# Kernel optimization log

Measured on AMD Instinct MI355X. Metric: run time of the kernel, lower is better.

The kernel has to match this reference:

```python
import jax, jax.numpy as jnp
import numpy as np

L, B, E = 512, 32, 512
ENC_HID, DEC_HID = 512, 1024
H2 = 2 * ENC_HID            # bidirectional encoder output dim
OUT_DIM = 32000             # generation (trg) vocab
CPY_LEN = 60000             # copy vocab size (embedding rows / prediction cols)
SRC_V = 50000
NEG = -1e10


def setup_inputs() -> dict:
    key = jax.random.key(0)
    ks = jax.random.split(key, 20)
    s = 0.02
    f32 = jnp.float32
    return {
        "src": jax.random.randint(ks[0], (L, B), 0, SRC_V),
        "inp": jax.random.randint(ks[1], (B,), 0, CPY_LEN),
        "hidden": jax.random.normal(ks[2], (2, B, DEC_HID), f32),
        "c": jax.random.normal(ks[3], (2, B, DEC_HID), f32),
        "encoder_outputs": jax.random.normal(ks[4], (L, B, H2), f32),
        "mask": jnp.ones((B, L), jnp.int32),
        "selective_weights": jax.random.normal(ks[5], (B, L - 2), f32),
        "src_to_cpy": jax.random.randint(ks[6], (SRC_V,), 0, CPY_LEN),
        # learned parameters
        "emb": jax.random.normal(ks[7], (CPY_LEN, E), f32) * s,
        "W_attn": jax.random.normal(ks[8], (H2 + DEC_HID, DEC_HID), f32) * s,
        "b_attn": jnp.zeros((DEC_HID,), f32),
        "v_attn": jax.random.normal(ks[9], (DEC_HID,), f32) * s,
        "W_ih0": jax.random.normal(ks[10], (4 * DEC_HID, 2 * H2 + E), f32) * s,
        "W_hh0": jax.random.normal(ks[11], (4 * DEC_HID, DEC_HID), f32) * s,
        "b_ih0": jnp.zeros((4 * DEC_HID,), f32),
        "b_hh0": jnp.zeros((4 * DEC_HID,), f32),
        "W_ih1": jax.random.normal(ks[12], (4 * DEC_HID, DEC_HID), f32) * s,
        "W_hh1": jax.random.normal(ks[13], (4 * DEC_HID, DEC_HID), f32) * s,
        "b_ih1": jnp.zeros((4 * DEC_HID,), f32),
        "b_hh1": jnp.zeros((4 * DEC_HID,), f32),
        "W_fc": jax.random.normal(ks[14], (OUT_DIM, H2 + DEC_HID + E), f32) * s,
        "b_fc": jnp.zeros((OUT_DIM,), f32),
        "W_copy": jax.random.normal(ks[15], (DEC_HID, H2), f32) * s,
        "b_copy": jnp.zeros((DEC_HID,), f32),
    }


def _lstm_cell(x, h, c, W_ih, W_hh, b_ih, b_hh):
    # PyTorch gate order: i, f, g, o
    g = x @ W_ih.T + h @ W_hh.T + b_ih + b_hh
    i, f, gg, o = jnp.split(g, 4, axis=-1)
    c_new = jax.nn.sigmoid(f) * c + jax.nn.sigmoid(i) * jnp.tanh(gg)
    h_new = jax.nn.sigmoid(o) * jnp.tanh(c_new)
    return h_new, c_new


def reference(src, inp, hidden, c, encoder_outputs, mask, selective_weights,
              src_to_cpy, emb, W_attn, b_attn, v_attn,
              W_ih0, W_hh0, b_ih0, b_hh0, W_ih1, W_hh1, b_ih1, b_hh1,
              W_fc, b_fc, W_copy, b_copy):
    Bn = encoder_outputs.shape[1]
    Ln = encoder_outputs.shape[0]
    # update_selective_weights: mask where converted src token != prev prediction, softmax
    conv_src = src_to_cpy[src[1:-1]]              # [L-2, B]
    copy_mask = (conv_src == inp[None, :]).T      # [B, L-2]
    sel = jnp.where(copy_mask, selective_weights, NEG)
    sel = jax.nn.softmax(sel, axis=1)             # [B, L-2]
    embedded = emb[inp]                           # [B, E] (dropout in eval mode = identity)
    enc = jnp.transpose(encoder_outputs, (1, 0, 2))  # [B, L, H2]
    # Bahdanau attention over encoder outputs
    h_top = hidden[-1]                            # [B, D]
    h_rep = jnp.broadcast_to(h_top[:, None, :], (Bn, Ln, h_top.shape[-1]))
    energy = jnp.tanh(jnp.concatenate([h_rep, enc], axis=2) @ W_attn + b_attn)  # [B, L, D]
    scores = energy @ v_attn                      # [B, L]
    scores = jnp.where(mask == 0, NEG, scores)
    attn_w = jax.nn.softmax(scores, axis=1)
    attentive_read = jnp.einsum('bl,blh->bh', attn_w, enc)        # [B, H2]
    sel = jnp.where(mask[:, 1:-1] == 0, NEG, sel)                 # faithful second mask
    selective_read = jnp.einsum('bl,blh->bh', sel, enc[:, 1:-1])  # [B, H2]
    # 2-layer LSTM, single step
    x = jnp.concatenate([embedded, attentive_read, selective_read], axis=1)
    h0, c0 = _lstm_cell(x, hidden[0], c[0], W_ih0, W_hh0, b_ih0, b_hh0)
    h1, c1 = _lstm_cell(h0, hidden[1], c[1], W_ih1, W_hh1, b_ih1, b_hh1)
    hidden_new = jnp.stack([h0, h1])
    c_new = jnp.stack([c0, c1])
    # generation scores
    gen = jnp.concatenate([h1, attentive_read, embedded], axis=1) @ W_fc.T + b_fc  # [B, OUT_DIM]
    # copy scores over trimmed source positions
    proj = jnp.tanh(enc[:, 1:-1] @ W_copy.T + b_copy)             # [B, L-2, D]
    copy_scores = jnp.einsum('bld,bd->bl', proj, h1)              # [B, L-2]
    copy_scores = jnp.where(mask[:, 1:-1] == 0, NEG, copy_scores)
    # assemble predictions: generation slice + indexed scatter of copy scores
    src_cpy = src_to_cpy[src.T[:, 1:-1]]                          # [B, L-2]
    preds = jnp.zeros((Bn, CPY_LEN), gen.dtype)
    preds = preds.at[:, :OUT_DIM].set(gen)
    preds = preds.at[jnp.arange(Bn)[:, None], src_cpy].set(copy_scores)
    return preds, hidden_new, c_new, attn_w, copy_scores
```

## Files before the change

### kernel.cpp

```cpp
#include <hip/hip_runtime.h>
#include <stdint.h>

typedef unsigned short u16;
typedef unsigned int   u32;
typedef __attribute__((ext_vector_type(8))) short short8;
typedef __attribute__((ext_vector_type(4))) float f32x4;

#define NEGF (-1.0e10f)

static constexpr int LL = 512, BB = 32, EE = 512, H2 = 1024, DH = 1024;
static constexpr int KX = 2560, OUTD = 32000, CPY = 60000;

static constexpr size_t HID_OFF   = 1920000;
static constexpr size_t C_OFF     = HID_OFF + 65536;
static constexpr size_t ATTN_OFF  = C_OFF + 65536;
static constexpr size_t CS_OFF    = ATTN_OFF + 16384;

static constexpr size_t WS_ENC    = 0;
static constexpr size_t WS_WA1T   = 33554432;
static constexpr size_t WS_WA2T   = 35651584;
static constexpr size_t WS_WCT    = 37748736;
static constexpr size_t WS_HPF    = 39845888;
static constexpr size_t WS_SCORES = 39976960;
static constexpr size_t WS_CSACC  = 40042496;
static constexpr size_t WS_SELP   = 40108032;
static constexpr size_t WS_XBF    = 40173568;
static constexpr size_t WS_GENBF  = 40337408;
static constexpr size_t WS_H0PBF  = 40501248;
static constexpr size_t WS_H1PBF  = 40566784;
static constexpr size_t WS_H0NBF  = 40632320;
static constexpr size_t WS_GATES  = 40697856;
static constexpr size_t WS_H1     = 41222144;
static constexpr size_t WS_TOTAL  = 41353216;
static constexpr size_t WS_GPART  = WS_WA1T;
static constexpr size_t WS_TAG    = WS_ENC;

__device__ __forceinline__ u16 f2bf(float x){
  u32 u = __builtin_bit_cast(u32, x);
  u32 r = (u + 0x7FFFu + ((u >> 16) & 1u)) >> 16;
  return (u16)r;
}
__device__ __forceinline__ float bf2f(u16 h){
  u32 u = ((u32)h) << 16; return __builtin_bit_cast(float, u);
}
__device__ __forceinline__ float fsig(float x){ return 1.f/(1.f + __expf(-x)); }
__device__ __forceinline__ float ftanh(float x){
  float e = __expf(2.f*x);
  return 1.f - 2.f/(e + 1.f);
}

#define GLDS16(gp, lp) __builtin_amdgcn_global_load_lds( \
    (__attribute__((address_space(1))) void*)(gp), \
    (__attribute__((address_space(3))) void*)(lp), 16, 0, 0)

__global__ void k_f32_to_bf16(const float* __restrict__ in, u16* __restrict__ out, int n4){
  int stride = gridDim.x * blockDim.x;
  for (int i = blockIdx.x*blockDim.x + threadIdx.x; i < n4; i += stride){
    float4 v = ((const float4*)in)[i];
    u32 lo = (u32)f2bf(v.x) | ((u32)f2bf(v.y) << 16);
    u32 hi = (u32)f2bf(v.z) | ((u32)f2bf(v.w) << 16);
    ((uint2*)out)[i] = make_uint2(lo, hi);
  }
}

__global__ void k_wattn_t(const float* __restrict__ W, u16* __restrict__ wa1t, u16* __restrict__ wa2t){
  __shared__ float Tt[64*65];
  int n0 = blockIdx.x*64, k0 = blockIdx.y*64;
  int t = threadIdx.x;
  int nn = t & 63, kq = t >> 6;
  for (int kk = kq; kk < 64; kk += 4)
    Tt[kk*65 + nn] = W[(size_t)(k0+kk)*1024 + n0 + nn];
  __syncthreads();
  u16* dst = (k0 < 1024) ? wa1t : wa2t;
  int kbase = (k0 < 1024) ? k0 : (k0 - 1024);
  int kk2 = t & 63, nq = t >> 6;
  for (int nn2 = nq; nn2 < 64; nn2 += 4)
    dst[(size_t)(n0+nn2)*1024 + kbase + kk2] = f2bf(Tt[kk2*65 + nn2]);
}

__global__ void k_prep(const int* __restrict__ src, const int* __restrict__ inp,
                       const float* __restrict__ hidden, const float* __restrict__ selw,
                       const int* __restrict__ s2c, const float* __restrict__ emb,
                       const int* __restrict__ mask,
                       u16* __restrict__ xbf, u16* __restrict__ genbf,
                       u16* __restrict__ h0pbf, u16* __restrict__ h1pbf,
                       float* __restrict__ scores, float* __restrict__ csacc,
                       float* __restrict__ selp)
{
  int b = blockIdx.x, t = threadIdx.x;
  int ib = inp[b];
  for (int h = t; h < 512; h += 256){
    u16 e = f2bf(emb[(size_t)ib*512 + h]);
    xbf[b*2560 + h] = e;
    genbf[b*2560 + 2048 + h] = e;
  }
  for (int k = t; k < 1024; k += 256){
    h0pbf[b*1024 + k] = f2bf(hidden[b*1024 + k]);
    h1pbf[b*1024 + k] = f2bf(hidden[32768 + b*1024 + k]);
  }
  for (int l = t; l < 512; l += 256){
    scores[b*512 + l] = 0.f;
    csacc[b*512 + l] = 0.f;
  }
  __shared__ float red[256];
  float lg[2];
  #pragma unroll
  for (int i = 0; i < 2; ++i){
    int j = t + i*256;
    lg[i] = NEGF;
    if (j < 510){
      int cs = s2c[src[(j+1)*32 + b]];
      if (cs == ib) lg[i] = selw[b*510 + j];
    }
  }
  red[t] = fmaxf(lg[0], lg[1]); __syncthreads();
  for (int s = 128; s > 0; s >>= 1){ if (t < s) red[t] = fmaxf(red[t], red[t+s]); __syncthreads(); }
  float mx = red[0]; __syncthreads();
  float e0 = (t < 510)     ? __expf(lg[0] - mx) : 0.f;
  float e1 = (t+256 < 510) ? __expf(lg[1] - mx) : 0.f;
  red[t] = e0 + e1; __syncthreads();
  for (int s = 128; s > 0; s >>= 1){ if (t < s) red[t] += red[t+s]; __syncthreads(); }
  float inv = 1.f / red[0];
  #pragma unroll
  for (int i = 0; i < 2; ++i){
    int j = t + i*256;
    if (j < 510){
      float v = ((i == 0) ? e0 : e1) * inv;
      int l = j + 1;
      selp[b*512 + l] = (mask[b*512 + l] != 0) ? v : NEGF;
    }
  }
}

__launch_bounds__(256)
__global__ void k_mfma(const u16* __restrict__ A, int lda, int Mvalid,
                       const u16* __restrict__ Bmat, int ldb, int K,
                       const float* __restrict__ preadd, int spa,
                       const float* __restrict__ dotw, int sdw,
                       float* __restrict__ dotout, int Ldot, int skipedge,
                       float* __restrict__ outstore, int NT)
{
  __shared__ u16 As[128*64];
  __shared__ u16 Bs[128*64];
  int nwg = gridDim.x, bid = blockIdx.x;
  int q = nwg >> 3, r = nwg & 7, xc = bid & 7, ix = bid >> 3;
  int wg = (xc < r ? xc*(q+1) : r*(q+1) + (xc - r)*q) + ix;
  int mt = wg / NT, nt = wg % NT;
  int m0 = mt * 128, n0 = nt * 128;
  int tid = threadIdx.x, lane = tid & 63, wid = tid >> 6;
  int wm = wid >> 1, wn = wid & 1;

  f32x4 acc[4][4];
  #pragma unroll
  for (int i = 0; i < 4; ++i)
    #pragma unroll
    for (int j = 0; j < 4; ++j)
      acc[i][j] = (f32x4){0.f, 0.f, 0.f, 0.f};

  int srow = lane >> 3;
  int soff = ((lane & 7) ^ srow) * 8;

  for (int k0 = 0; k0 < K; k0 += 64){
    __syncthreads();
    #pragma unroll
    for (int j = 0; j < 4; ++j){
      int qq = wid*4 + j;
      int ra = m0 + qq*8 + srow; if (ra >= Mvalid) ra = Mvalid - 1;
      GLDS16(A + (size_t)ra*lda + k0 + soff, (char*)As + qq*1024 + lane*16);
      int rb = n0 + qq*8 + srow;
      GLDS16(Bmat + (size_t)rb*ldb + k0 + soff, (char*)Bs + qq*1024 + lane*16);
    }
    __syncthreads();
    #pragma unroll
    for (int kk = 0; kk < 2; ++kk){
      short8 af[4], bfr[4];
      #pragma unroll
      for (int mi = 0; mi < 4; ++mi){
        int rr = wm*64 + mi*16 + (lane & 15);
        int kb = (kk*64 + ((lane >> 4) << 4)) ^ ((rr & 7) << 4);
        af[mi] = *(const short8*)((const char*)As + rr*128 + kb);
      }
      #pragma unroll
      for (int nj = 0; nj < 4; ++nj){
        int rr = wn*64 + nj*16 + (lane & 15);
        int kb = (kk*64 + ((lane >> 4) << 4)) ^ ((rr & 7) << 4);
        bfr[nj] = *(const short8*)((const char*)Bs + rr*128 + kb);
      }
      #pragma unroll
      for (int mi = 0; mi < 4; ++mi)
        #pragma unroll
        for (int nj = 0; nj < 4; ++nj)
          acc[mi][nj] = __builtin_amdgcn_mfma_f32_16x16x32_bf16(af[mi], bfr[nj], acc[mi][nj], 0, 0, 0);
    }
  }

  int g = lane >> 4, cn = lane & 15;
  if (outstore){
    int Nld = NT * 128;
    #pragma unroll
    for (int mi = 0; mi < 4; ++mi)
      #pragma unroll
      for (int rr2 = 0; rr2 < 4; ++rr2){
        int row = m0 + wm*64 + mi*16 + g*4 + rr2;
        if (row < Mvalid){
          #pragma unroll
          for (int nj = 0; nj < 4; ++nj){
            int n = n0 + wn*64 + nj*16 + cn;
            outstore[(size_t)row*Nld + n] = acc[mi][nj][rr2] + preadd[(size_t)(row & 31)*spa + n];
          }
        }
      }
  } else {
    #pragma unroll
    for (int mi = 0; mi < 4; ++mi)
      #pragma unroll
      for (int rr2 = 0; rr2 < 4; ++rr2){
        int row = m0 + wm*64 + mi*16 + g*4 + rr2;
        int bb = row & 31;
        float part = 0.f;
        #pragma unroll
        for (int nj = 0; nj < 4; ++nj){
          int n = n0 + wn*64 + nj*16 + cn;
          float tv = ftanh(acc[mi][nj][rr2] + preadd[(size_t)bb*spa + n]);
          part = fmaf(tv, dotw[(size_t)bb*sdw + n], part);
        }
        part += __shfl_xor(part, 1);
        part += __shfl_xor(part, 2);
        part += __shfl_xor(part, 4);
        part += __shfl_xor(part, 8);
        if (cn == 0){
          int l = row >> 5;
          if (!skipedge || (l > 0 && l < Ldot - 1))
            atomicAdd(&dotout[(size_t)bb*Ldot + l], part);
        }
      }
  }
}

__global__ void k_softmax_attn(const float* __restrict__ scores, const int* __restrict__ mask,
                               float* __restrict__ attnw){
  int b = blockIdx.x, t = threadIdx.x;
  __shared__ float red[256];
  float v0 = scores[b*512 + t];
  float v1 = scores[b*512 + 256 + t];
  if (mask[b*512 + t] == 0) v0 = NEGF;
  if (mask[b*512 + 256 + t] == 0) v1 = NEGF;
  red[t] = fmaxf(v0, v1); __syncthreads();
  for (int s = 128; s > 0; s >>= 1){ if (t < s) red[t] = fmaxf(red[t], red[t+s]); __syncthreads(); }
  float mx = red[0]; __syncthreads();
  float e0 = __expf(v0 - mx), e1 = __expf(v1 - mx);
  red[t] = e0 + e1; __syncthreads();
  for (int s = 128; s > 0; s >>= 1){ if (t < s) red[t] += red[t+s]; __syncthreads(); }
  float inv = 1.f / red[0];
  attnw[b*512 + t] = e0 * inv;
  attnw[b*512 + 256 + t] = e1 * inv;
}

__global__ void k_reads(const u16* __restrict__ encbf, const float* __restrict__ attnw,
                        const float* __restrict__ selp,
                        u16* __restrict__ xbf, u16* __restrict__ genbf){
  int b = blockIdx.y;
  int h = blockIdx.x*128 + threadIdx.x;
  float aa = 0.f, as = 0.f;
  #pragma unroll 4
  for (int l = 0; l < 512; ++l){
    float e = bf2f(encbf[((size_t)l*32 + b)*1024 + h]);
    aa = fmaf(attnw[b*512 + l], e, aa);
    if (l >= 1 && l < 511) as = fmaf(selp[b*512 + l], e, as);
  }
  u16 ab = f2bf(aa);
  xbf[b*2560 + 512 + h]  = ab;
  xbf[b*2560 + 1536 + h] = f2bf(as);
  genbf[b*2560 + 1024 + h] = ab;
}

__launch_bounds__(256)
__global__ void k_wgemm(const float* __restrict__ W1, const u16* __restrict__ xb1, int K1,
                        const float* __restrict__ W2, const u16* __restrict__ xb2, int K2,
                        const float* __restrict__ bias1, const float* __restrict__ bias2,
                        float* __restrict__ outB, int ldo, int cps)
{
  __shared__ u16 As[64*64];
  __shared__ u16 Bs[32*64];
  const int tid = threadIdx.x, lane = tid & 63, w = tid >> 6;
  const int o0 = blockIdx.x * 64;
  const int c1 = K1 >> 6;
  const int c0 = blockIdx.y * cps;

  f32x4 acc[2];
  acc[0] = (f32x4){0.f,0.f,0.f,0.f};
  acc[1] = (f32x4){0.f,0.f,0.f,0.f};

  const int ar = tid >> 2, akq = (tid & 3) * 16;
  const int aswz = (ar & 7) << 4;
  const int brow = tid >> 3, pslot = tid & 7;
  const int lslot = pslot ^ (brow & 7);

  float4 aA[4], aB[4];

  auto aload = [&](int c, float4* dst){
    const float* Wp; int Kp, kc;
    if (c < c1){ Wp = W1; Kp = K1; kc = c << 6; }
    else       { Wp = W2; Kp = K2; kc = (c - c1) << 6; }
    const float4* p = (const float4*)(Wp + (size_t)(o0 + ar)*Kp + kc + akq);
    dst[0] = p[0]; dst[1] = p[1]; dst[2] = p[2]; dst[3] = p[3];
  };

  auto body = [&](int c, float4* cur, float4* nxt, bool more){
    asm volatile("s_waitcnt lgkmcnt(0)" ::: "memory");
    __builtin_amdgcn_s_barrier();
    {
      const u16* xp; int Kp, kc;
      if (c < c1){ xp = xb1; Kp = K1; kc = c << 6; }
      else       { xp = xb2; Kp = K2; kc = (c - c1) << 6; }
      GLDS16(xp + (size_t)brow*Kp + kc + lslot*8, (char*)Bs + tid*16);
    }
    u32 p0 = (u32)f2bf(cur[0].x) | ((u32)f2bf(cur[0].y) << 16);
    u32 p1 = (u32)f2bf(cur[0].z) | ((u32)f2bf(cur[0].w) << 16);
    u32 p2 = (u32)f2bf(cur[1].x) | ((u32)f2bf(cur[1].y) << 16);
    u32 p3 = (u32)f2bf(cur[1].z) | ((u32)f2bf(cur[1].w) << 16);
    u32 p4 = (u32)f2bf(cur[2].x) | ((u32)f2bf(cur[2].y) << 16);
    u32 p5 = (u32)f2bf(cur[2].z) | ((u32)f2bf(cur[2].w) << 16);
    u32 p6 = (u32)f2bf(cur[3].x) | ((u32)f2bf(cur[3].y) << 16);
    u32 p7 = (u32)f2bf(cur[3].z) | ((u32)f2bf(cur[3].w) << 16);
    char* rowp = (char*)As + ar*128;
    *(uint4*)(rowp + ((akq*2)      ^ aswz)) = make_uint4(p0,p1,p2,p3);
    *(uint4*)(rowp + ((akq*2 + 16) ^ aswz)) = make_uint4(p4,p5,p6,p7);
    asm volatile("s_waitcnt lgkmcnt(0)\n\ts_waitcnt vmcnt(0)" ::: "memory");
    __builtin_amdgcn_s_barrier();
    if (more) aload(c + 1, nxt);
    #pragma unroll
    for (int kk = 0; kk < 2; ++kk){
      int rrA = w*16 + (lane & 15);
      int kb  = kk*64 + ((lane >> 4) << 4);
      short8 af = *(const short8*)((const char*)As + rrA*128 + (kb ^ ((rrA & 7) << 4)));
      #pragma unroll
      for (int nj = 0; nj < 2; ++nj){
        int rrB = nj*16 + (lane & 15);
        short8 bfv = *(const short8*)((const char*)Bs + rrB*128 + (kb ^ ((rrB & 7) << 4)));
        acc[nj] = __builtin_amdgcn_mfma_f32_16x16x32_bf16(af, bfv, acc[nj], 0, 0, 0);
      }
    }
  };

  aload(c0, aA);
  for (int li = 0; li < cps; li += 2){
    body(c0 + li,     aA, aB, true);
    body(c0 + li + 1, aB, aA, (li + 2) < cps);
  }

  int g = lane >> 4, cn = lane & 15;
  int ob = o0 + w*16 + g*4;
  float* outP = outB + (size_t)blockIdx.y * 32 * (size_t)ldo;
  float4 badd = make_float4(0.f,0.f,0.f,0.f);
  if (blockIdx.y == 0){
    if (bias1){ float4 t = *(const float4*)(bias1 + ob);
      badd.x += t.x; badd.y += t.y; badd.z += t.z; badd.w += t.w; }
    if (bias2){ float4 t = *(const float4*)(bias2 + ob);
      badd.x += t.x; badd.y += t.y; badd.z += t.z; badd.w += t.w; }
  }
  #pragma unroll
  for (int nj = 0; nj < 2; ++nj){
    int bcol = nj*16 + cn;
    float4 v = make_float4(acc[nj][0] + badd.x, acc[nj][1] + badd.y,
                           acc[nj][2] + badd.z, acc[nj][3] + badd.w);
    *(float4*)(outP + (size_t)bcol*ldo + ob) = v;
  }
}

__global__ void k_gred(const float* __restrict__ part, float* __restrict__ g){
  int i = blockIdx.x*256 + threadIdx.x;
  g[i] = part[i] + part[131072 + i] + part[262144 + i] + part[393216 + i];
}

__global__ void k_cell(const float* __restrict__ g, const float* __restrict__ c_in,
                       float* __restrict__ h_out, float* __restrict__ c_out,
                       u16* __restrict__ hbf, int hld, float* __restrict__ h_plain){
  int idx = blockIdx.x*256 + threadIdx.x;
  int b = idx >> 10, j = idx & 1023;
  const float* gb = g + (size_t)b*4096;
  float gi = gb[j];
  float gf = gb[1024 + j];
  float gg = gb[2048 + j];
  float go = gb[3072 + j];
  float cv = c_in[b*1024 + j];
  float cnv = fsig(gf)*cv + fsig(gi)*ftanh(gg);
  float hn  = fsig(go)*ftanh(cnv);
  c_out[b*1024 + j] = cnv;
  h_out[b*1024 + j] = hn;
  hbf[(size_t)b*hld + j] = f2bf(hn);
  if (h_plain) h_plain[b*1024 + j] = hn;
}

__global__ void k_zerotail(float* __restrict__ preds){
  int i = blockIdx.x*256 + threadIdx.x;
  if (i < 224000){
    int b = i / 7000, t = i % 7000;
    ((float4*)(preds + (size_t)b*CPY + OUTD))[t] = make_float4(0.f, 0.f, 0.f, 0.f);
  }
}

__global__ void k_csfinal(const float* __restrict__ csacc, const int* __restrict__ mask,
                          float* __restrict__ cs_out){
  int i = blockIdx.x*256 + threadIdx.x;
  if (i < 16320){
    int b = i / 510, j = i % 510, l = j + 1;
    cs_out[b*510 + j] = (mask[b*512 + l] != 0) ? csacc[b*512 + l] : NEGF;
  }
}

__global__ void k_tag_init(const int* __restrict__ src, const int* __restrict__ s2c,
                           int* __restrict__ tag){
  int i = blockIdx.x*256 + threadIdx.x;
  if (i < 16320){
    int b = i / 510, j = i % 510;
    tag[(size_t)b*CPY + s2c[src[(j+1)*32 + b]]] = -1;
  }
}
__global__ void k_tag_max(const int* __restrict__ src, const int* __restrict__ s2c,
                          int* __restrict__ tag){
  int i = blockIdx.x*256 + threadIdx.x;
  if (i < 16320){
    int b = i / 510, j = i % 510;
    atomicMax(&tag[(size_t)b*CPY + s2c[src[(j+1)*32 + b]]], j);
  }
}
__global__ void k_tag_write(const int* __restrict__ src, const int* __restrict__ s2c,
                            const int* __restrict__ tag, const float* __restrict__ cs,
                            float* __restrict__ preds){
  int i = blockIdx.x*256 + threadIdx.x;
  if (i < 16320){
    int b = i / 510, j = i % 510;
    int idx = s2c[src[(j+1)*32 + b]];
    if (tag[(size_t)b*CPY + idx] == j)
      preds[(size_t)b*CPY + idx] = cs[b*510 + j];
  }
}

extern "C" void kernel_launch(void* const* d_in, const int* in_sizes, int n_in,
                              void* d_out, int out_size, void* d_ws, size_t ws_size,
                              hipStream_t stream){
  const int*   src    = (const int*)  d_in[0];
  const int*   inp    = (const int*)  d_in[1];
  const float* hidden = (const float*)d_in[2];
  const float* cst    = (const float*)d_in[3];
  const float* enc    = (const float*)d_in[4];
  const int*   mask   = (const int*)  d_in[5];
  const float* selw   = (const float*)d_in[6];
  const int*   s2c    = (const int*)  d_in[7];
  const float* emb    = (const float*)d_in[8];
  const float* W_attn = (const float*)d_in[9];
  const float* b_attn = (const float*)d_in[10];
  const float* v_attn = (const float*)d_in[11];
  const float* W_ih0  = (const float*)d_in[12];
  const float* W_hh0  = (const float*)d_in[13];
  const float* b_ih0  = (const float*)d_in[14];
  const float* b_hh0  = (const float*)d_in[15];
  const float* W_ih1  = (const float*)d_in[16];
  const float* W_hh1  = (const float*)d_in[17];
  const float* b_ih1  = (const float*)d_in[18];
  const float* b_hh1  = (const float*)d_in[19];
  const float* W_fc   = (const float*)d_in[20];
  const float* b_fc   = (const float*)d_in[21];
  const float* W_copy = (const float*)d_in[22];
  const float* b_copy = (const float*)d_in[23];

  if (ws_size < WS_TOTAL) return;

  float* out = (float*)d_out;
  char*  ws  = (char*)d_ws;
  u16*   encbf  = (u16*)  (ws + WS_ENC);
  u16*   wa1t   = (u16*)  (ws + WS_WA1T);
  u16*   wa2t   = (u16*)  (ws + WS_WA2T);
  u16*   wct    = (u16*)  (ws + WS_WCT);
  float* hpf    = (float*)(ws + WS_HPF);
  float* scores = (float*)(ws + WS_SCORES);
  float* csacc  = (float*)(ws + WS_CSACC);
  float* selp   = (float*)(ws + WS_SELP);
  u16*   xbf    = (u16*)  (ws + WS_XBF);
  u16*   genbf  = (u16*)  (ws + WS_GENBF);
  u16*   h0pbf  = (u16*)  (ws + WS_H0PBF);
  u16*   h1pbf  = (u16*)  (ws + WS_H1PBF);
  u16*   h0nbf  = (u16*)  (ws + WS_H0NBF);
  float* gates  = (float*)(ws + WS_GATES);
  float* gpart  = (float*)(ws + WS_GPART);
  float* h1     = (float*)(ws + WS_H1);
  int*   tag    = (int*)  (ws + WS_TAG);

  k_f32_to_bf16<<<2048, 256, 0, stream>>>(enc,    encbf, (LL*BB*H2)/4);
  k_f32_to_bf16<<<512,  256, 0, stream>>>(W_copy, wct,   (DH*H2)/4);
  k_wattn_t<<<dim3(16, 32), 256, 0, stream>>>(W_attn, wa1t, wa2t);
  k_prep<<<32, 256, 0, stream>>>(src, inp, hidden, selw, s2c, emb, mask,
                                 xbf, genbf, h0pbf, h1pbf, scores, csacc, selp);

  k_mfma<<<8, 256, 0, stream>>>(h1pbf, 1024, 32, wa1t, 1024, 1024,
                                b_attn, 0, nullptr, 0, nullptr, 512, 0, hpf, 8);
  k_mfma<<<1024, 256, 0, stream>>>(encbf, 1024, LL*BB, wa2t, 1024, 1024,
                                   hpf, 1024, v_attn, 0, scores, 512, 0, nullptr, 8);
  k_softmax_attn<<<32, 256, 0, stream>>>(scores, mask, out + ATTN_OFF);
  k_reads<<<dim3(8, 32), 128, 0, stream>>>(encbf, out + ATTN_OFF, selp, xbf, genbf);

  k_wgemm<<<dim3(64, 4), 256, 0, stream>>>(W_ih0, xbf, KX, W_hh0, h0pbf, DH,
                                           b_ih0, b_hh0, gpart, 4096, 14);
  k_gred<<<512, 256, 0, stream>>>(gpart, gates);
  k_cell<<<128, 256, 0, stream>>>(gates, cst, out + HID_OFF, out + C_OFF,
                                  h0nbf, 1024, nullptr);
  k_wgemm<<<dim3(64, 4), 256, 0, stream>>>(W_ih1, h0nbf, DH, W_hh1, h1pbf, DH,
                                           b_ih1, b_hh1, gpart, 4096, 8);
  k_gred<<<512, 256, 0, stream>>>(gpart, gates);
  k_cell<<<128, 256, 0, stream>>>(gates, cst + 32768, out + HID_OFF + 32768,
                                  out + C_OFF + 32768, genbf, 2560, h1);

  k_mfma<<<1024, 256, 0, stream>>>(encbf, 1024, LL*BB, wct, 1024, 1024,
                                   b_copy, 0, h1, 1024, csacc, 512, 1, nullptr, 8);

  k_wgemm<<<dim3(500, 1), 256, 0, stream>>>(W_fc, genbf, KX, nullptr, nullptr, 0,
                                            b_fc, nullptr, out, CPY, 40);
  k_zerotail<<<875, 256, 0, stream>>>(out);
  k_csfinal<<<64, 256, 0, stream>>>(csacc, mask, out + CS_OFF);

  k_tag_init <<<64, 256, 0, stream>>>(src, s2c, tag);
  k_tag_max  <<<64, 256, 0, stream>>>(src, s2c, tag);
  k_tag_write<<<64, 256, 0, stream>>>(src, s2c, tag, out + CS_OFF, out);
}
```

Measured before the change: 397.6 us.

## Double-buffer GEMM LDS staging, fuse gate reduction and tag init, split reads

The MFMA GEMM switches from single-buffered 64-wide K tiles to double-buffered 32-wide K tiles with a new XOR swizzle, so the next tile's global-to-LDS load overlaps the current tile's compute. The weight GEMM gets the same treatment: its activation tile is double-buffered and the next weight loads are issued before the current tile is converted. The gate partial-sum reduction kernel is folded into the LSTM cell kernel, and copy-score finalisation is merged with tag initialisation, which removes several launches. The attention/selective read kernel now splits the sequence across two thread halves and combines them through shared memory, giving more parallelism. The cost is more LDS per block and one barrier per 32-wide K step instead of two per 64-wide step.

After: 395.6 us. Within noise of the previous version (-0.5%).

```diff
diff --git a/kernel.cpp b/kernel.cpp
--- a/kernel.cpp
+++ b/kernel.cpp
@@ -29,7 +29,6 @@
 static constexpr size_t WS_H0PBF  = 40501248;
 static constexpr size_t WS_H1PBF  = 40566784;
 static constexpr size_t WS_H0NBF  = 40632320;
-static constexpr size_t WS_GATES  = 40697856;
 static constexpr size_t WS_H1     = 41222144;
 static constexpr size_t WS_TOTAL  = 41353216;
 static constexpr size_t WS_GPART  = WS_WA1T;
@@ -140,8 +139,8 @@
                        float* __restrict__ dotout, int Ldot, int skipedge,
                        float* __restrict__ outstore, int NT)
 {
-  __shared__ u16 As[128*64];
-  __shared__ u16 Bs[128*64];
+  __shared__ u16 As[2][128*32];
+  __shared__ u16 Bs[2][128*32];
   int nwg = gridDim.x, bid = blockIdx.x;
   int q = nwg >> 3, r = nwg & 7, xc = bid & 7, ix = bid >> 3;
   int wg = (xc < r ? xc*(q+1) : r*(q+1) + (xc - r)*q) + ix;
@@ -157,41 +156,46 @@
     for (int j = 0; j < 4; ++j)
       acc[i][j] = (f32x4){0.f, 0.f, 0.f, 0.f};
 
-  int srow = lane >> 3;
-  int soff = ((lane & 7) ^ srow) * 8;
-
-  for (int k0 = 0; k0 < K; k0 += 64){
+  int r0 = tid >> 2,          s0 = tid & 3;
+  int r1 = (tid + 256) >> 2;
+  int xv0 = (r0 ^ (r0 >> 2)) & 3, xv1 = (r1 ^ (r1 >> 2)) & 3;
+  int sc0 = (s0 ^ xv0) << 3,      sc1 = (s0 ^ xv1) << 3;
+  int raA0 = m0 + r0; if (raA0 >= Mvalid) raA0 = Mvalid - 1;
+  int raA1 = m0 + r1; if (raA1 >= Mvalid) raA1 = Mvalid - 1;
+  int rbB0 = n0 + r0, rbB1 = n0 + r1;
+
+  auto stage = [&](int k0, u16* asb, u16* bsb){
+    GLDS16(A    + (size_t)raA0*lda + k0 + sc0, (char*)asb + tid*16);
+    GLDS16(A    + (size_t)raA1*lda + k0 + sc1, (char*)asb + (tid+256)*16);
+    GLDS16(Bmat + (size_t)rbB0*ldb + k0 + sc0, (char*)bsb + tid*16);
+    GLDS16(Bmat + (size_t)rbB1*ldb + k0 + sc1, (char*)bsb + (tid+256)*16);
+  };
+
+  int KT = K >> 5;
+  stage(0, As[0], Bs[0]);
+  for (int kt = 0; kt < KT; ++kt){
     __syncthreads();
-    #pragma unroll
-    for (int j = 0; j < 4; ++j){
-      int qq = wid*4 + j;
-      int ra = m0 + qq*8 + srow; if (ra >= Mvalid) ra = Mvalid - 1;
-      GLDS16(A + (size_t)ra*lda + k0 + soff, (char*)As + qq*1024 + lane*16);
-      int rb = n0 + qq*8 + srow;
-      GLDS16(Bmat + (size_t)rb*ldb + k0 + soff, (char*)Bs + qq*1024 + lane*16);
+    if (kt + 1 < KT) stage((kt+1) << 5, As[(kt+1) & 1], Bs[(kt+1) & 1]);
+    const char* ap = (const char*)As[kt & 1];
+    const char* bp = (const char*)Bs[kt & 1];
+    short8 af[4], bfr[4];
+    #pragma unroll
+    for (int mi = 0; mi < 4; ++mi){
+      int rr = wm*64 + mi*16 + (lane & 15);
+      int xv = (rr ^ (rr >> 2)) & 3;
+      af[mi] = *(const short8*)(ap + rr*64 + (((lane >> 4) ^ xv) << 4));
     }
-    __syncthreads();
-    #pragma unroll
-    for (int kk = 0; kk < 2; ++kk){
-      short8 af[4], bfr[4];
+    #pragma unroll
+    for (int nj = 0; nj < 4; ++nj){
+      int rr = wn*64 + nj*16 + (lane & 15);
+      int xv = (rr ^ (rr >> 2)) & 3;
+      bfr[nj] = *(const short8*)(bp + rr*64 + (((lane >> 4) ^ xv) << 4));
+    }
+    #pragma unroll
+    for (int mi = 0; mi < 4; ++mi)
       #pragma unroll
-      for (int mi = 0; mi < 4; ++mi){
-        int rr = wm*64 + mi*16 + (lane & 15);
-        int kb = (kk*64 + ((lane >> 4) << 4)) ^ ((rr & 7) << 4);
-        af[mi] = *(const short8*)((const char*)As + rr*128 + kb);
-      }
-      #pragma unroll
-      for (int nj = 0; nj < 4; ++nj){
-        int rr = wn*64 + nj*16 + (lane & 15);
-        int kb = (kk*64 + ((lane >> 4) << 4)) ^ ((rr & 7) << 4);
-        bfr[nj] = *(const short8*)((const char*)Bs + rr*128 + kb);
-      }
-      #pragma unroll
-      for (int mi = 0; mi < 4; ++mi)
-        #pragma unroll
-        for (int nj = 0; nj < 4; ++nj)
-          acc[mi][nj] = __builtin_amdgcn_mfma_f32_16x16x32_bf16(af[mi], bfr[nj], acc[mi][nj], 0, 0, 0);
-    }
+      for (int nj = 0; nj < 4; ++nj)
+        acc[mi][nj] = __builtin_amdgcn_mfma_f32_16x16x32_bf16(af[mi], bfr[nj], acc[mi][nj], 0, 0, 0);
   }
 
   int g = lane >> 4, cn = lane & 15;
@@ -260,18 +264,28 @@
                         const float* __restrict__ selp,
                         u16* __restrict__ xbf, u16* __restrict__ genbf){
   int b = blockIdx.y;
-  int h = blockIdx.x*128 + threadIdx.x;
+  int tid = threadIdx.x;
+  int h = blockIdx.x*256 + (tid & 255);
+  int lh = tid >> 8;
   float aa = 0.f, as = 0.f;
+  int l0 = lh*256, l1 = l0 + 256;
   #pragma unroll 4
-  for (int l = 0; l < 512; ++l){
+  for (int l = l0; l < l1; ++l){
     float e = bf2f(encbf[((size_t)l*32 + b)*1024 + h]);
     aa = fmaf(attnw[b*512 + l], e, aa);
     if (l >= 1 && l < 511) as = fmaf(selp[b*512 + l], e, as);
   }
-  u16 ab = f2bf(aa);
-  xbf[b*2560 + 512 + h]  = ab;
-  xbf[b*2560 + 1536 + h] = f2bf(as);
-  genbf[b*2560 + 1024 + h] = ab;
+  __shared__ float red[512][2];
+  red[tid][0] = aa; red[tid][1] = as;
+  __syncthreads();
+  if (tid < 256){
+    aa = red[tid][0] + red[tid+256][0];
+    as = red[tid][1] + red[tid+256][1];
+    u16 ab = f2bf(aa);
+    xbf[b*2560 + 512 + h]    = ab;
+    xbf[b*2560 + 1536 + h]   = f2bf(as);
+    genbf[b*2560 + 1024 + h] = ab;
+  }
 }
 
 __launch_bounds__(256)
@@ -281,7 +295,7 @@
                         float* __restrict__ outB, int ldo, int cps)
 {
   __shared__ u16 As[64*64];
-  __shared__ u16 Bs[32*64];
+  __shared__ u16 Bs[2][32*64];
   const int tid = threadIdx.x, lane = tid & 63, w = tid >> 6;
   const int o0 = blockIdx.x * 64;
   const int c1 = K1 >> 6;
@@ -305,16 +319,16 @@
     const float4* p = (const float4*)(Wp + (size_t)(o0 + ar)*Kp + kc + akq);
     dst[0] = p[0]; dst[1] = p[1]; dst[2] = p[2]; dst[3] = p[3];
   };
-
-  auto body = [&](int c, float4* cur, float4* nxt, bool more){
-    asm volatile("s_waitcnt lgkmcnt(0)" ::: "memory");
-    __builtin_amdgcn_s_barrier();
-    {
-      const u16* xp; int Kp, kc;
-      if (c < c1){ xp = xb1; Kp = K1; kc = c << 6; }
-      else       { xp = xb2; Kp = K2; kc = (c - c1) << 6; }
-      GLDS16(xp + (size_t)brow*Kp + kc + lslot*8, (char*)Bs + tid*16);
-    }
+  auto bstage = [&](int c, u16* bsb){
+    const u16* xp; int Kp, kc;
+    if (c < c1){ xp = xb1; Kp = K1; kc = c << 6; }
+    else       { xp = xb2; Kp = K2; kc = (c - c1) << 6; }
+    GLDS16(xp + (size_t)brow*Kp + kc + lslot*8, (char*)bsb + tid*16);
+  };
+
+  auto body = [&](int c, float4* cur, float4* nxt, const u16* bsCur, u16* bsNxt, bool more){
+    __syncthreads();
+    if (more){ aload(c + 1, nxt); bstage(c + 1, bsNxt); }
     u32 p0 = (u32)f2bf(cur[0].x) | ((u32)f2bf(cur[0].y) << 16);
     u32 p1 = (u32)f2bf(cur[0].z) | ((u32)f2bf(cur[0].w) << 16);
     u32 p2 = (u32)f2bf(cur[1].x) | ((u32)f2bf(cur[1].y) << 16);
@@ -326,9 +340,8 @@
     char* rowp = (char*)As + ar*128;
     *(uint4*)(rowp + ((akq*2)      ^ aswz)) = make_uint4(p0,p1,p2,p3);
     *(uint4*)(rowp + ((akq*2 + 16) ^ aswz)) = make_uint4(p4,p5,p6,p7);
-    asm volatile("s_waitcnt lgkmcnt(0)\n\ts_waitcnt vmcnt(0)" ::: "memory");
+    asm volatile("s_waitcnt lgkmcnt(0)" ::: "memory");
     __builtin_amdgcn_s_barrier();
-    if (more) aload(c + 1, nxt);
     #pragma unroll
     for (int kk = 0; kk < 2; ++kk){
       int rrA = w*16 + (lane & 15);
@@ -337,16 +350,16 @@
       #pragma unroll
       for (int nj = 0; nj < 2; ++nj){
         int rrB = nj*16 + (lane & 15);
-        short8 bfv = *(const short8*)((const char*)Bs + rrB*128 + (kb ^ ((rrB & 7) << 4)));
+        short8 bfv = *(const short8*)((const char*)bsCur + rrB*128 + (kb ^ ((rrB & 7) << 4)));
         acc[nj] = __builtin_amdgcn_mfma_f32_16x16x32_bf16(af, bfv, acc[nj], 0, 0, 0);
       }
     }
   };
 
-  aload(c0, aA);
+  aload(c0, aA); bstage(c0, Bs[0]);
   for (int li = 0; li < cps; li += 2){
-    body(c0 + li,     aA, aB, true);
-    body(c0 + li + 1, aB, aA, (li + 2) < cps);
+    body(c0 + li,     aA, aB, Bs[0], Bs[1], true);
+    body(c0 + li + 1, aB, aA, Bs[1], Bs[0], (li + 2) < cps);
   }
 
   int g = lane >> 4, cn = lane & 15;
@@ -368,21 +381,20 @@
   }
 }
 
-__global__ void k_gred(const float* __restrict__ part, float* __restrict__ g){
-  int i = blockIdx.x*256 + threadIdx.x;
-  g[i] = part[i] + part[131072 + i] + part[262144 + i] + part[393216 + i];
-}
-
-__global__ void k_cell(const float* __restrict__ g, const float* __restrict__ c_in,
+__global__ void k_cell(const float* __restrict__ gpart, const float* __restrict__ c_in,
                        float* __restrict__ h_out, float* __restrict__ c_out,
                        u16* __restrict__ hbf, int hld, float* __restrict__ h_plain){
   int idx = blockIdx.x*256 + threadIdx.x;
   int b = idx >> 10, j = idx & 1023;
-  const float* gb = g + (size_t)b*4096;
-  float gi = gb[j];
-  float gf = gb[1024 + j];
-  float gg = gb[2048 + j];
-  float go = gb[3072 + j];
+  float gi = 0.f, gf = 0.f, gg = 0.f, go = 0.f;
+  #pragma unroll
+  for (int p = 0; p < 4; ++p){
+    const float* gb = gpart + (size_t)p*131072 + (size_t)b*4096;
+    gi += gb[j];
+    gf += gb[1024 + j];
+    gg += gb[2048 + j];
+    go += gb[3072 + j];
+  }
   float cv = c_in[b*1024 + j];
   float cnv = fsig(gf)*cv + fsig(gi)*ftanh(gg);
   float hn  = fsig(go)*ftanh(cnv);
@@ -400,20 +412,13 @@
   }
 }
 
-__global__ void k_csfinal(const float* __restrict__ csacc, const int* __restrict__ mask,
-                          float* __restrict__ cs_out){
+__global__ void k_cstag(const float* __restrict__ csacc, const int* __restrict__ mask,
+                        const int* __restrict__ src, const int* __restrict__ s2c,
+                        float* __restrict__ cs_out, int* __restrict__ tag){
   int i = blockIdx.x*256 + threadIdx.x;
   if (i < 16320){
     int b = i / 510, j = i % 510, l = j + 1;
     cs_out[b*510 + j] = (mask[b*512 + l] != 0) ? csacc[b*512 + l] : NEGF;
-  }
-}
-
-__global__ void k_tag_init(const int* __restrict__ src, const int* __restrict__ s2c,
-                           int* __restrict__ tag){
-  int i = blockIdx.x*256 + threadIdx.x;
-  if (i < 16320){
-    int b = i / 510, j = i % 510;
     tag[(size_t)b*CPY + s2c[src[(j+1)*32 + b]]] = -1;
   }
 }
@@ -482,7 +487,6 @@
   u16*   h0pbf  = (u16*)  (ws + WS_H0PBF);
   u16*   h1pbf  = (u16*)  (ws + WS_H1PBF);
   u16*   h0nbf  = (u16*)  (ws + WS_H0NBF);
-  float* gates  = (float*)(ws + WS_GATES);
   float* gpart  = (float*)(ws + WS_GPART);
   float* h1     = (float*)(ws + WS_H1);
   int*   tag    = (int*)  (ws + WS_TAG);
@@ -498,17 +502,15 @@
   k_mfma<<<1024, 256, 0, stream>>>(encbf, 1024, LL*BB, wa2t, 1024, 1024,
                                    hpf, 1024, v_attn, 0, scores, 512, 0, nullptr, 8);
   k_softmax_attn<<<32, 256, 0, stream>>>(scores, mask, out + ATTN_OFF);
-  k_reads<<<dim3(8, 32), 128, 0, stream>>>(encbf, out + ATTN_OFF, selp, xbf, genbf);
+  k_reads<<<dim3(4, 32), 512, 0, stream>>>(encbf, out + ATTN_OFF, selp, xbf, genbf);
 
   k_wgemm<<<dim3(64, 4), 256, 0, stream>>>(W_ih0, xbf, KX, W_hh0, h0pbf, DH,
                                            b_ih0, b_hh0, gpart, 4096, 14);
-  k_gred<<<512, 256, 0, stream>>>(gpart, gates);
-  k_cell<<<128, 256, 0, stream>>>(gates, cst, out + HID_OFF, out + C_OFF,
+  k_cell<<<128, 256, 0, stream>>>(gpart, cst, out + HID_OFF, out + C_OFF,
                                   h0nbf, 1024, nullptr);
   k_wgemm<<<dim3(64, 4), 256, 0, stream>>>(W_ih1, h0nbf, DH, W_hh1, h1pbf, DH,
                                            b_ih1, b_hh1, gpart, 4096, 8);
-  k_gred<<<512, 256, 0, stream>>>(gpart, gates);
-  k_cell<<<128, 256, 0, stream>>>(gates, cst + 32768, out + HID_OFF + 32768,
+  k_cell<<<128, 256, 0, stream>>>(gpart, cst + 32768, out + HID_OFF + 32768,
                                   out + C_OFF + 32768, genbf, 2560, h1);
 
   k_mfma<<<1024, 256, 0, stream>>>(encbf, 1024, LL*BB, wct, 1024, 1024,
@@ -517,9 +519,8 @@
   k_wgemm<<<dim3(500, 1), 256, 0, stream>>>(W_fc, genbf, KX, nullptr, nullptr, 0,
                                             b_fc, nullptr, out, CPY, 40);
   k_zerotail<<<875, 256, 0, stream>>>(out);
-  k_csfinal<<<64, 256, 0, stream>>>(csacc, mask, out + CS_OFF);
-
-  k_tag_init <<<64, 256, 0, stream>>>(src, s2c, tag);
-  k_tag_max  <<<64, 256, 0, stream>>>(src, s2c, tag);
+
+  k_cstag   <<<64, 256, 0, stream>>>(csacc, mask, src, s2c, out + CS_OFF, tag);
+  k_tag_max <<<64, 256, 0, stream>>>(src, s2c, tag);
   k_tag_write<<<64, 256, 0, stream>>>(src, s2c, tag, out + CS_OFF, out);
 }
```
